# Optimization experiments

Measured on AMD Instinct MI355X. Metric: run time of the kernel, lower is better.

## Reference

```python
import jax, jax.numpy as jnp
import numpy as np

B, T, D = 32, 2048, 128


def setup_inputs() -> dict:
    key = jax.random.key(0)
    k1, k2, k3 = jax.random.split(key, 3)
    values = jax.random.normal(k1, (B, T, D), dtype=jnp.float32)
    # monotonically increasing per-feature timestamps (irregular sampling)
    times = jnp.cumsum(jax.random.uniform(k2, (B, T, D), dtype=jnp.float32), axis=1)
    mask = jax.random.randint(k3, (B, T, D), 0, 2) > 0  # True = observed
    return {"values": values, "times": times, "mask": mask}


def _fill(x, t, mask):
    """Parallel forward fill (LOCF) and backward fill (NOCB) of x and t.

    Replaces the serial Keras RNN scan with cummax/cummin over observation
    indices followed by a gather. Matches ForwardCell semantics:
      forward : x init 0, t init times[:, 0, :]
      backward: x init 0, t init max(times, axis=1)
    """
    Tn = x.shape[1]
    ar = jnp.broadcast_to(jnp.arange(Tn, dtype=jnp.int32)[None, :, None], x.shape)
    # ---- forward fill ----
    fidx = jax.lax.cummax(jnp.where(mask, ar, -1), axis=1)  # last observed idx
    fvalid = fidx >= 0
    fi = jnp.clip(fidx, 0, Tn - 1)
    x_last = jnp.where(fvalid, jnp.take_along_axis(x, fi, axis=1), 0.0)
    t_last = jnp.where(fvalid, jnp.take_along_axis(t, fi, axis=1), t[:, :1, :])
    # ---- backward fill ----
    bidx = jax.lax.cummin(jnp.where(mask, ar, Tn), axis=1, reverse=True)  # next observed idx
    bvalid = bidx < Tn
    bi = jnp.clip(bidx, 0, Tn - 1)
    x_next = jnp.where(bvalid, jnp.take_along_axis(x, bi, axis=1), 0.0)
    t_next = jnp.where(bvalid, jnp.take_along_axis(t, bi, axis=1),
                       jnp.max(t, axis=1, keepdims=True))
    return x_last, t_last, x_next, t_next


def reference(values, times, mask):
    x_last, t_last, x_next, t_next = _fill(values, times, mask)
    denom = t_next - t_last
    num = x_last * (t_next - times) + x_next * (times - t_last)
    safe = denom != 0.0
    x_itp = num / jnp.where(safe, denom, 1.0)
    x_itp = jnp.where(safe & jnp.isfinite(x_itp), x_itp, 0.0)  # nan/inf -> 0
    return jnp.where(mask, values, x_itp)
```

## Files before the change

kernel.cpp:

```cpp
#include <hip/hip_runtime.h>
#include <math.h>

constexpr int B   = 32;
constexpr int T   = 2048;
constexpr int D   = 128;
constexpr int CS  = 8;
constexpr int RT  = 8;
constexpr int BT  = RT * CS;
constexpr int PAD = 129;

__global__ __launch_bounds__(256)
void interp_xchg_kernel(const float* __restrict__ values,
                        const float* __restrict__ times,
                        const int*   __restrict__ mask,
                        float*       __restrict__ out)
{
    __shared__ float    SLV[RT][PAD];
    __shared__ float    SLT[RT][PAD];
    __shared__ float    SFV[RT][PAD];
    __shared__ float    SFT[RT][PAD];
    __shared__ unsigned SM [RT][PAD];

    const int tid = threadIdx.x;
    const int d4  = tid & 31;
    const int row = tid >> 5;
    const int d0  = d4 << 2;

    const int blk = blockIdx.x;
    const int b   = blk >> 5;
    const int tb  = blk & 31;
    const int bt0 = tb * BT;
    const int t0  = bt0 + row * CS;

    const size_t bbase = (size_t)b * T * D;
    const float* vrow = values + bbase + (size_t)t0 * D + d0;
    const float* trow = times  + bbase + (size_t)t0 * D + d0;
    const int*   mrow = mask   + bbase + (size_t)t0 * D + d0;

    float vv[CS][4], tt[CS][4];
    unsigned mb[4] = {0u, 0u, 0u, 0u};
#pragma unroll
    for (int i = 0; i < CS; ++i) {
        const float4 a = *reinterpret_cast<const float4*>(vrow + i * D);
        const float4 s = *reinterpret_cast<const float4*>(trow + i * D);
        const int4   m = *reinterpret_cast<const int4*>(mrow + i * D);
        vv[i][0] = a.x; vv[i][1] = a.y; vv[i][2] = a.z; vv[i][3] = a.w;
        tt[i][0] = s.x; tt[i][1] = s.y; tt[i][2] = s.z; tt[i][3] = s.w;
        mb[0] |= (m.x != 0 ? 1u : 0u) << i;
        mb[1] |= (m.y != 0 ? 1u : 0u) << i;
        mb[2] |= (m.z != 0 ? 1u : 0u) << i;
        mb[3] |= (m.w != 0 ? 1u : 0u) << i;
    }

    unsigned pb[4] = {0u, 0u, 0u, 0u};
    unsigned nb[4] = {0u, 0u, 0u, 0u};
    if (row == 0 && bt0 > 0) {
#pragma unroll
        for (int k = 0; k < 16; ++k) {
            const int st = bt0 - 16 + k;
            const int4 m = *reinterpret_cast<const int4*>(
                mask + bbase + (size_t)st * D + d0);
            pb[0] |= (m.x != 0 ? 1u : 0u) << k;
            pb[1] |= (m.y != 0 ? 1u : 0u) << k;
            pb[2] |= (m.z != 0 ? 1u : 0u) << k;
            pb[3] |= (m.w != 0 ? 1u : 0u) << k;
        }
    }
    if (row == RT - 1 && bt0 + BT < T) {
#pragma unroll
        for (int k = 0; k < 16; ++k) {
            const int st = bt0 + BT + k;
            const int4 m = *reinterpret_cast<const int4*>(
                mask + bbase + (size_t)st * D + d0);
            nb[0] |= (m.x != 0 ? 1u : 0u) << k;
            nb[1] |= (m.y != 0 ? 1u : 0u) << k;
            nb[2] |= (m.z != 0 ? 1u : 0u) << k;
            nb[3] |= (m.w != 0 ? 1u : 0u) << k;
        }
    }

#pragma unroll
    for (int j = 0; j < 4; ++j) {
        float lv = 0.f, lt = 0.f, fv = 0.f, ft = 0.f;
#pragma unroll
        for (int i = 0; i < CS; ++i)
            if ((mb[j] >> i) & 1u) { lv = vv[i][j]; lt = tt[i][j]; }
#pragma unroll
        for (int i = CS - 1; i >= 0; --i)
            if ((mb[j] >> i) & 1u) { fv = vv[i][j]; ft = tt[i][j]; }
        const int d = d0 + j;
        SLV[row][d] = lv; SLT[row][d] = lt;
        SFV[row][d] = fv; SFT[row][d] = ft;
        SM [row][d] = mb[j];
    }
    __syncthreads();

    float res[CS][4];
#pragma unroll
    for (int j = 0; j < 4; ++j) {
        const int d = d0 + j;

        float cfx = 0.f, cft = 0.f;
        bool have = false;
        for (int r = row - 1; r >= 0; --r) {
            if (SM[r][d]) { cfx = SLV[r][d]; cft = SLT[r][d]; have = true; break; }
        }
        if (!have && pb[j]) {
            const int st = bt0 - 16 + (31 - __builtin_clz(pb[j]));
            const size_t o = bbase + (size_t)st * D + d;
            cfx = values[o]; cft = times[o]; have = true;
        }
        if (!have) {
            const int start = (row == 0) ? (bt0 - 17) : (bt0 - 1);
            for (int st = start; st >= 0; --st) {
                if (mask[bbase + (size_t)st * D + d] != 0) {
                    const size_t o = bbase + (size_t)st * D + d;
                    cfx = values[o]; cft = times[o]; have = true; break;
                }
            }
        }
        if (!have) { cfx = 0.f; cft = times[bbase + d]; }

        float cbx = 0.f, cbt = 0.f;
        bool haveb = false;
        for (int r = row + 1; r < RT; ++r) {
            if (SM[r][d]) { cbx = SFV[r][d]; cbt = SFT[r][d]; haveb = true; break; }
        }
        if (!haveb && nb[j]) {
            const int st = bt0 + BT + __builtin_ctz(nb[j]);
            const size_t o = bbase + (size_t)st * D + d;
            cbx = values[o]; cbt = times[o]; haveb = true;
        }
        if (!haveb) {
            const int start = bt0 + BT + ((row == RT - 1) ? 16 : 0);
            for (int st = start; st < T; ++st) {
                if (mask[bbase + (size_t)st * D + d] != 0) {
                    const size_t o = bbase + (size_t)st * D + d;
                    cbx = values[o]; cbt = times[o]; haveb = true; break;
                }
            }
        }
        if (!haveb) { cbx = 0.f; cbt = times[bbase + (size_t)(T - 1) * D + d]; }

        float xl[CS], tl_[CS];
#pragma unroll
        for (int i = 0; i < CS; ++i) {
            if ((mb[j] >> i) & 1u) { cfx = vv[i][j]; cft = tt[i][j]; }
            xl[i] = cfx; tl_[i] = cft;
        }
#pragma unroll
        for (int i = CS - 1; i >= 0; --i) {
            const bool obs = (mb[j] >> i) & 1u;
            if (obs) { cbx = vv[i][j]; cbt = tt[i][j]; }
            const float denom = cbt - tl_[i];
            const float num   = xl[i] * (cbt - tt[i][j]) + cbx * (tt[i][j] - tl_[i]);
            const bool  safe  = (denom != 0.f);
            float xi = num / (safe ? denom : 1.f);
            xi = (safe && isfinite(xi)) ? xi : 0.f;
            res[i][j] = obs ? vv[i][j] : xi;
        }
    }

    float* orow = out + bbase + (size_t)t0 * D + d0;
#pragma unroll
    for (int i = 0; i < CS; ++i) {
        float4 o; o.x = res[i][0]; o.y = res[i][1]; o.z = res[i][2]; o.w = res[i][3];
        *reinterpret_cast<float4*>(orow + i * D) = o;
    }
}

extern "C" void kernel_launch(void* const* d_in, const int* in_sizes, int n_in,
                              void* d_out, int out_size, void* d_ws, size_t ws_size,
                              hipStream_t stream)
{
    const float* values = (const float*)d_in[0];
    const float* times  = (const float*)d_in[1];
    const int*   mask   = (const int*)d_in[2];
    float*       out    = (float*)d_out;

    const int blocks = B * (T / BT);
    interp_xchg_kernel<<<blocks, 256, 0, stream>>>(values, times, mask, out);
}
```

Baseline: 145.1 us.

## Replace shared-memory row exchange with wave-level shuffles and bitmask scans

Each 64-lane wave now handles a 64-row by 32-feature tile, so the cross-row carry exchange is done with __shfl and bitmask leading/trailing-bit searches instead of shared-memory arrays and a __syncthreads. The per-row serial search over previous rows becomes a clz/ctz on a packed observation bitmask. This removes LDS traffic and block-level barriers. Memory access narrows to 32-float (128-byte) row segments per wave rather than full 512-byte rows, which may affect coalescing.

After: 154.6 us. +6.6%, slower.

```diff
diff --git a/kernel.cpp b/kernel.cpp
--- a/kernel.cpp
+++ b/kernel.cpp
@@ -1,34 +1,30 @@
 #include <hip/hip_runtime.h>
 #include <math.h>
 
-constexpr int B   = 32;
-constexpr int T   = 2048;
-constexpr int D   = 128;
-constexpr int CS  = 8;
-constexpr int RT  = 8;
-constexpr int BT  = RT * CS;
-constexpr int PAD = 129;
+constexpr int B  = 32;
+constexpr int T  = 2048;
+constexpr int D  = 128;
+constexpr int CS = 8;
+constexpr int RT = 8;
+constexpr int BT = RT * CS;
+constexpr int DQ = 32;
 
 __global__ __launch_bounds__(256)
-void interp_xchg_kernel(const float* __restrict__ values,
+void interp_wave_kernel(const float* __restrict__ values,
                         const float* __restrict__ times,
                         const int*   __restrict__ mask,
                         float*       __restrict__ out)
 {
-    __shared__ float    SLV[RT][PAD];
-    __shared__ float    SLT[RT][PAD];
-    __shared__ float    SFV[RT][PAD];
-    __shared__ float    SFT[RT][PAD];
-    __shared__ unsigned SM [RT][PAD];
+    const int tid  = threadIdx.x;
+    const int lane = tid & 63;
+    const int row  = lane >> 3;
+    const int dg   = lane & 7;
+    const int waveId = (blockIdx.x << 2) + (tid >> 6);
+    const int dq = waveId & 3;
+    const int tb = (waveId >> 2) & 31;
+    const int b  = waveId >> 7;
 
-    const int tid = threadIdx.x;
-    const int d4  = tid & 31;
-    const int row = tid >> 5;
-    const int d0  = d4 << 2;
-
-    const int blk = blockIdx.x;
-    const int b   = blk >> 5;
-    const int tb  = blk & 31;
+    const int d0  = dq * DQ + dg * 4;
     const int bt0 = tb * BT;
     const int t0  = bt0 + row * CS;
 
@@ -52,95 +48,114 @@
         mb[3] |= (m.w != 0 ? 1u : 0u) << i;
     }
 
-    unsigned pb[4] = {0u, 0u, 0u, 0u};
-    unsigned nb[4] = {0u, 0u, 0u, 0u};
-    if (row == 0 && bt0 > 0) {
+    unsigned pbp0 = 0u, pbp1 = 0u;
+    unsigned nbp0 = 0u, nbp1 = 0u;
+    if (row == 0 && tb > 0) {
 #pragma unroll
         for (int k = 0; k < 16; ++k) {
-            const int st = bt0 - 16 + k;
             const int4 m = *reinterpret_cast<const int4*>(
-                mask + bbase + (size_t)st * D + d0);
-            pb[0] |= (m.x != 0 ? 1u : 0u) << k;
-            pb[1] |= (m.y != 0 ? 1u : 0u) << k;
-            pb[2] |= (m.z != 0 ? 1u : 0u) << k;
-            pb[3] |= (m.w != 0 ? 1u : 0u) << k;
+                mask + bbase + (size_t)(bt0 - 16 + k) * D + d0);
+            pbp0 |= (m.x != 0 ? 1u : 0u) << k;
+            pbp0 |= (m.y != 0 ? 1u : 0u) << (16 + k);
+            pbp1 |= (m.z != 0 ? 1u : 0u) << k;
+            pbp1 |= (m.w != 0 ? 1u : 0u) << (16 + k);
         }
     }
-    if (row == RT - 1 && bt0 + BT < T) {
+    if (row == RT - 1 && tb < 31) {
 #pragma unroll
         for (int k = 0; k < 16; ++k) {
-            const int st = bt0 + BT + k;
             const int4 m = *reinterpret_cast<const int4*>(
-                mask + bbase + (size_t)st * D + d0);
-            nb[0] |= (m.x != 0 ? 1u : 0u) << k;
-            nb[1] |= (m.y != 0 ? 1u : 0u) << k;
-            nb[2] |= (m.z != 0 ? 1u : 0u) << k;
-            nb[3] |= (m.w != 0 ? 1u : 0u) << k;
+                mask + bbase + (size_t)(bt0 + BT + k) * D + d0);
+            nbp0 |= (m.x != 0 ? 1u : 0u) << k;
+            nbp0 |= (m.y != 0 ? 1u : 0u) << (16 + k);
+            nbp1 |= (m.z != 0 ? 1u : 0u) << k;
+            nbp1 |= (m.w != 0 ? 1u : 0u) << (16 + k);
         }
     }
 
+    float lv[4], lt[4], fv[4], ftm[4];
 #pragma unroll
     for (int j = 0; j < 4; ++j) {
-        float lv = 0.f, lt = 0.f, fv = 0.f, ft = 0.f;
+        float a = 0.f, c = 0.f, e = 0.f, g = 0.f;
 #pragma unroll
         for (int i = 0; i < CS; ++i)
-            if ((mb[j] >> i) & 1u) { lv = vv[i][j]; lt = tt[i][j]; }
+            if ((mb[j] >> i) & 1u) { a = vv[i][j]; c = tt[i][j]; }
 #pragma unroll
         for (int i = CS - 1; i >= 0; --i)
-            if ((mb[j] >> i) & 1u) { fv = vv[i][j]; ft = tt[i][j]; }
-        const int d = d0 + j;
-        SLV[row][d] = lv; SLT[row][d] = lt;
-        SFV[row][d] = fv; SFT[row][d] = ft;
-        SM [row][d] = mb[j];
+            if ((mb[j] >> i) & 1u) { e = vv[i][j]; g = tt[i][j]; }
+        lv[j] = a; lt[j] = c; fv[j] = e; ftm[j] = g;
     }
-    __syncthreads();
+    const unsigned smP = (mb[0] & 0xFFu) | ((mb[1] & 0xFFu) << 8)
+                       | ((mb[2] & 0xFFu) << 16) | ((mb[3] & 0xFFu) << 24);
 
-    float res[CS][4];
+    unsigned allm[RT];
+#pragma unroll
+    for (int r = 0; r < RT; ++r)
+        allm[r] = (unsigned)__shfl((int)smP, r * 8 + dg, 64);
+    const unsigned pbs0 = (unsigned)__shfl((int)pbp0, dg, 64);
+    const unsigned pbs1 = (unsigned)__shfl((int)pbp1, dg, 64);
+    const unsigned nbs0 = (unsigned)__shfl((int)nbp0, 56 + dg, 64);
+    const unsigned nbs1 = (unsigned)__shfl((int)nbp1, 56 + dg, 64);
+
 #pragma unroll
     for (int j = 0; j < 4; ++j) {
         const int d = d0 + j;
+        unsigned rm = 0u;
+#pragma unroll
+        for (int r = 0; r < RT; ++r)
+            rm |= (((allm[r] >> (8 * j)) & 0xFFu) ? 1u : 0u) << r;
 
-        float cfx = 0.f, cft = 0.f;
-        bool have = false;
-        for (int r = row - 1; r >= 0; --r) {
-            if (SM[r][d]) { cfx = SLV[r][d]; cft = SLT[r][d]; have = true; break; }
-        }
-        if (!have && pb[j]) {
-            const int st = bt0 - 16 + (31 - __builtin_clz(pb[j]));
-            const size_t o = bbase + (size_t)st * D + d;
-            cfx = values[o]; cft = times[o]; have = true;
-        }
-        if (!have) {
-            const int start = (row == 0) ? (bt0 - 17) : (bt0 - 1);
-            for (int st = start; st >= 0; --st) {
-                if (mask[bbase + (size_t)st * D + d] != 0) {
-                    const size_t o = bbase + (size_t)st * D + d;
-                    cfx = values[o]; cft = times[o]; have = true; break;
+        const unsigned below = rm & ((1u << row) - 1u);
+        const unsigned above = rm >> (row + 1);
+
+        const int rs = below ? (31 - __builtin_clz(below)) : 0;
+        const int rb = above ? (row + 1 + __builtin_ctz(above)) : 0;
+        const float gLV = __shfl(lv[j],  rs * 8 + dg, 64);
+        const float gLT = __shfl(lt[j],  rs * 8 + dg, 64);
+        const float gFV = __shfl(fv[j],  rb * 8 + dg, 64);
+        const float gFT = __shfl(ftm[j], rb * 8 + dg, 64);
+
+        float cfx, cft;
+        if (below) { cfx = gLV; cft = gLT; }
+        else {
+            const unsigned pbj = ((j & 1) ? ((j < 2 ? pbs0 : pbs1) >> 16)
+                                          :  (j < 2 ? pbs0 : pbs1)) & 0xFFFFu;
+            if (pbj) {
+                const int st = bt0 - 16 + (31 - __builtin_clz(pbj));
+                const size_t o = bbase + (size_t)st * D + d;
+                cfx = values[o]; cft = times[o];
+            } else {
+                bool found = false; cfx = 0.f; cft = 0.f;
+                for (int st = bt0 - 17; st >= 0; --st) {
+                    if (mask[bbase + (size_t)st * D + d] != 0) {
+                        const size_t o = bbase + (size_t)st * D + d;
+                        cfx = values[o]; cft = times[o]; found = true; break;
+                    }
                 }
+                if (!found) { cfx = 0.f; cft = times[bbase + d]; }
             }
         }
-        if (!have) { cfx = 0.f; cft = times[bbase + d]; }
 
-        float cbx = 0.f, cbt = 0.f;
-        bool haveb = false;
-        for (int r = row + 1; r < RT; ++r) {
-            if (SM[r][d]) { cbx = SFV[r][d]; cbt = SFT[r][d]; haveb = true; break; }
-        }
-        if (!haveb && nb[j]) {
-            const int st = bt0 + BT + __builtin_ctz(nb[j]);
-            const size_t o = bbase + (size_t)st * D + d;
-            cbx = values[o]; cbt = times[o]; haveb = true;
-        }
-        if (!haveb) {
-            const int start = bt0 + BT + ((row == RT - 1) ? 16 : 0);
-            for (int st = start; st < T; ++st) {
-                if (mask[bbase + (size_t)st * D + d] != 0) {
-                    const size_t o = bbase + (size_t)st * D + d;
-                    cbx = values[o]; cbt = times[o]; haveb = true; break;
+        float cbx, cbt;
+        if (above) { cbx = gFV; cbt = gFT; }
+        else {
+            const unsigned nbj = ((j & 1) ? ((j < 2 ? nbs0 : nbs1) >> 16)
+                                          :  (j < 2 ? nbs0 : nbs1)) & 0xFFFFu;
+            if (nbj) {
+                const int st = bt0 + BT + __builtin_ctz(nbj);
+                const size_t o = bbase + (size_t)st * D + d;
+                cbx = values[o]; cbt = times[o];
+            } else {
+                bool found = false; cbx = 0.f; cbt = 0.f;
+                for (int st = bt0 + BT + 16; st < T; ++st) {
+                    if (mask[bbase + (size_t)st * D + d] != 0) {
+                        const size_t o = bbase + (size_t)st * D + d;
+                        cbx = values[o]; cbt = times[o]; found = true; break;
+                    }
                 }
+                if (!found) { cbx = 0.f; cbt = times[bbase + (size_t)(T - 1) * D + d]; }
             }
         }
-        if (!haveb) { cbx = 0.f; cbt = times[bbase + (size_t)(T - 1) * D + d]; }
 
         float xl[CS], tl_[CS];
 #pragma unroll
@@ -157,14 +172,14 @@
             const bool  safe  = (denom != 0.f);
             float xi = num / (safe ? denom : 1.f);
             xi = (safe && isfinite(xi)) ? xi : 0.f;
-            res[i][j] = obs ? vv[i][j] : xi;
+            vv[i][j] = obs ? vv[i][j] : xi;
         }
     }
 
     float* orow = out + bbase + (size_t)t0 * D + d0;
 #pragma unroll
     for (int i = 0; i < CS; ++i) {
-        float4 o; o.x = res[i][0]; o.y = res[i][1]; o.z = res[i][2]; o.w = res[i][3];
+        float4 o; o.x = vv[i][0]; o.y = vv[i][1]; o.z = vv[i][2]; o.w = vv[i][3];
         *reinterpret_cast<float4*>(orow + i * D) = o;
     }
 }
@@ -178,6 +193,6 @@
     const int*   mask   = (const int*)d_in[2];
     float*       out    = (float*)d_out;
 
-    const int blocks = B * (T / BT);
-    interp_xchg_kernel<<<blocks, 256, 0, stream>>>(values, times, mask, out);
+    const int blocks = (B * (T / BT) * (D / DQ)) / 4;
+    interp_wave_kernel<<<blocks, 256, 0, stream>>>(values, times, mask, out);
 }
```
